# Optimization experiments

Hardware: AMD Instinct MI355X
Metric: run time of the kernel (lower is better)

The kernel has to match this reference:

```python
import jax, jax.numpy as jnp
import numpy as np

H = 64  # lstm_units
FORGET_BIAS = 1.0  # TF LSTMCell default


def setup_inputs() -> dict:
    key = jax.random.key(0)
    k1, k2, k3 = jax.random.split(key, 3)
    B, T = 256, 2048
    x = jax.random.normal(k1, (B, T, 1), dtype=jnp.float32)
    # Layer 1: LSTMCell(64), input dim 1 -> kernel [(1+64), 4*64]
    W1 = jax.random.normal(k2, (1 + H, 4 * H), dtype=jnp.float32) * 0.1
    b1 = jnp.zeros((4 * H,), dtype=jnp.float32)
    # Layer 2: LSTMCell(1), input dim 64 -> kernel [(64+1), 4*1]
    W2 = jax.random.normal(k3, (H + 1, 4), dtype=jnp.float32) * 0.1
    b2 = jnp.zeros((4,), dtype=jnp.float32)
    return {"x": x, "W1": W1, "b1": b1, "W2": W2, "b2": b2}


def _lstm_step(c, h, xt, W, b):
    # TF LSTMCell: gates from concat([x, h]) @ W + b, order i, j, f, o
    z = jnp.concatenate([xt, h], axis=-1) @ W + b
    i, j, f, o = jnp.split(z, 4, axis=-1)
    c_new = jax.nn.sigmoid(f + FORGET_BIAS) * c + jax.nn.sigmoid(i) * jnp.tanh(j)
    h_new = jax.nn.sigmoid(o) * jnpp_tanh(c_new) if False else jax.nn.sigmoid(o) * jnp.tanh(c_new)
    return c_new, h_new


def reference(x, W1, b1, W2, b2):
    # x: [B, T, 1] -> outputs of 2-layer stacked LSTM, final layer size 1
    B = x.shape[0]

    def step(carry, xt):
        c1, h1, c2, h2 = carry
        c1, h1 = _lstm_step(c1, h1, xt, W1, b1)
        c2, h2 = _lstm_step(c2, h2, h1, W2, b2)
        return (c1, h1, c2, h2), h2

    init = (
        jnp.zeros((B, H), x.dtype),
        jnp.zeros((B, H), x.dtype),
        jnp.zeros((B, 1), x.dtype),
        jnp.zeros((B, 1), x.dtype),
    )
    x_tbf = jnp.swapaxes(x, 0, 1)  # [T, B, 1]
    _, ys = jax.lax.scan(step, init, x_tbf)  # ys: [T, B, 1]
    return jnp.swapaxes(ys, 0, 1)  # [B, T, 1]
```

## Files before the change

kernel.cpp:

```cpp
#include <hip/hip_runtime.h>

constexpr int kT = 2048;
constexpr int kB = 256;
constexpr int kH = 64;

__device__ __forceinline__ float fast_sig(float x) {
    return __builtin_amdgcn_rcpf(1.0f + __expf(-x));
}
__device__ __forceinline__ float fast_tanh(float x) {
    float t = __expf(2.0f * x);
    return 1.0f - 2.0f * __builtin_amdgcn_rcpf(t + 1.0f);
}
__device__ __forceinline__ float bcast(float v, int lane) {
    return __int_as_float(__builtin_amdgcn_readlane(__float_as_int(v), lane));
}

__global__ __launch_bounds__(320)
__attribute__((amdgpu_waves_per_eu(1)))
void lstm2_kernel(
    const float* __restrict__ x, const float* __restrict__ W1,
    const float* __restrict__ b1, const float* __restrict__ W2,
    const float* __restrict__ b2, float* __restrict__ out)
{
    __shared__ float4 x4_lds[kT / 4];
    __shared__ float4 out4_lds[kT / 4];
    __shared__ float h1_lds[2][kH];
    float* x_lds = (float*)x4_lds;
    float* out_lds = (float*)out4_lds;

    const int tid = threadIdx.x;
    const int b = blockIdx.x;
    const float4* xg4 = (const float4*)(x + (size_t)b * kT);
    float4* outg4 = (float4*)(out + (size_t)b * kT);

    for (int i = tid; i < kT / 4; i += 320) x4_lds[i] = xg4[i];
    if (tid < kH) { h1_lds[0][tid] = 0.0f; h1_lds[1][tid] = 0.0f; }

    const int w = tid >> 6;
    const int l = tid & 63;

    float w0 = 0.0f, b1g = 0.0f;
    float4 wh4[16];
    #pragma unroll
    for (int k = 0; k < 16; ++k) wh4[k] = make_float4(0.f, 0.f, 0.f, 0.f);
    float c1 = 0.0f;
    int u = 0, g = 0;

    float w2p0 = 0, w2p1 = 0, w2p2 = 0, w2p3 = 0;
    float4 w2t = {0, 0, 0, 0}, b2v = {0, 0, 0, 0};
    float c2 = 0.0f, h2 = 0.0f;
    float zi_s = 0, zj_s = 0, zf_s = 0, zo_s = 0;

    if (w < 4) {
        g = l >> 4;
        u = 16 * w + (l & 15);
        const int col = g * 64 + u;
        w0 = W1[col];
        b1g = b1[col];
        #pragma unroll
        for (int k = 0; k < 16; ++k) {
            wh4[k].x = W1[(4 * k + 1) * 256 + col];
            wh4[k].y = W1[(4 * k + 2) * 256 + col];
            wh4[k].z = W1[(4 * k + 3) * 256 + col];
            wh4[k].w = W1[(4 * k + 4) * 256 + col];
        }
    } else {
        const int s = l & 15, gg = l >> 4;
        w2p0 = W2[(s +  0) * 4 + gg];
        w2p1 = W2[(s + 16) * 4 + gg];
        w2p2 = W2[(s + 32) * 4 + gg];
        w2p3 = W2[(s + 48) * 4 + gg];
        w2t = ((const float4*)W2)[kH];
        b2v = ((const float4*)b2)[0];
    }

    #pragma unroll
    for (int k = 0; k < 16; ++k)
        asm volatile("" : "+v"(wh4[k].x), "+v"(wh4[k].y),
                          "+v"(wh4[k].z), "+v"(wh4[k].w));
    asm volatile("" : "+v"(w0), "+v"(b1g));
    asm volatile("" : "+v"(w2p0), "+v"(w2p1), "+v"(w2p2), "+v"(w2p3));
    asm volatile("" : "+v"(w2t.x), "+v"(w2t.y), "+v"(w2t.z), "+v"(w2t.w));
    asm volatile("" : "+v"(b2v.x), "+v"(b2v.y), "+v"(b2v.z), "+v"(b2v.w));

    __syncthreads();

    int cur = 0;
    for (int t = 0; t < kT; ++t) {
        const int nxt = cur ^ 1;
        if (w < 4) {
            const float xt = x_lds[t];
            const float hv = h1_lds[cur][l];
            float z0 = fmaf(xt, w0, b1g), z1 = 0.0f, z2 = 0.0f, z3 = 0.0f;
            #pragma unroll
            for (int k = 0; k < 16; ++k) {
                z0 = fmaf(bcast(hv, 4 * k + 0), wh4[k].x, z0);
                z1 = fmaf(bcast(hv, 4 * k + 1), wh4[k].y, z1);
                z2 = fmaf(bcast(hv, 4 * k + 2), wh4[k].z, z2);
                z3 = fmaf(bcast(hv, 4 * k + 3), wh4[k].w, z3);
            }
            float z = (z0 + z1) + (z2 + z3);
            float zz = (g == 1) ? 2.0f * z : ((g == 2) ? z + 1.0f : z);
            float sg = fast_sig(zz);
            float a = (g == 1) ? fmaf(2.0f, sg, -1.0f) : sg;
            const int base = l & 15;
            const float ai = __shfl(a, base);
            const float aj = __shfl(a, base + 16);
            const float af = __shfl(a, base + 32);
            const float ao = __shfl(a, base + 48);
            c1 = fmaf(af, c1, ai * aj);
            const float h1n = ao * fast_tanh(c1);
            if (g == 0) h1_lds[nxt][u] = h1n;
        } else {
            if (t >= 2) {
                const float zi = zi_s + h2 * w2t.x;
                const float zj = zj_s + h2 * w2t.y;
                const float zf = zf_s + h2 * w2t.z;
                const float zo = zo_s + h2 * w2t.w;
                c2 = fast_sig(zf + 1.0f) * c2 + fast_sig(zi) * fast_tanh(zj);
                h2 = fast_sig(zo) * fast_tanh(c2);
                if (l == 0) out_lds[t - 2] = h2;
            }
            if (t >= 1) {
                const int s = l & 15;
                const float* hb = h1_lds[cur];
                float p = hb[s] * w2p0;
                p = fmaf(hb[s + 16], w2p1, p);
                p = fmaf(hb[s + 32], w2p2, p);
                p = fmaf(hb[s + 48], w2p3, p);
                p += __shfl_xor(p, 1);
                p += __shfl_xor(p, 2);
                p += __shfl_xor(p, 4);
                p += __shfl_xor(p, 8);
                zi_s = __shfl(p, s)      + b2v.x;
                zj_s = __shfl(p, s + 16) + b2v.y;
                zf_s = __shfl(p, s + 32) + b2v.z;
                zo_s = __shfl(p, s + 48) + b2v.w;
            }
        }
        __syncthreads();
        cur = nxt;
    }

    if (w == 4) {
        {
            const float zi = zi_s + h2 * w2t.x;
            const float zj = zj_s + h2 * w2t.y;
            const float zf = zf_s + h2 * w2t.z;
            const float zo = zo_s + h2 * w2t.w;
            c2 = fast_sig(zf + 1.0f) * c2 + fast_sig(zi) * fast_tanh(zj);
            h2 = fast_sig(zo) * fast_tanh(c2);
            if (l == 0) out_lds[kT - 2] = h2;
        }
        {
            const int s = l & 15;
            const float* hb = h1_lds[cur];
            float p = hb[s] * w2p0;
            p = fmaf(hb[s + 16], w2p1, p);
            p = fmaf(hb[s + 32], w2p2, p);
            p = fmaf(hb[s + 48], w2p3, p);
            p += __shfl_xor(p, 1);
            p += __shfl_xor(p, 2);
            p += __shfl_xor(p, 4);
            p += __shfl_xor(p, 8);
            const float zi = __shfl(p, s)      + b2v.x + h2 * w2t.x;
            const float zj = __shfl(p, s + 16) + b2v.y + h2 * w2t.y;
            const float zf = __shfl(p, s + 32) + b2v.z + h2 * w2t.z;
            const float zo = __shfl(p, s + 48) + b2v.w + h2 * w2t.w;
            c2 = fast_sig(zf + 1.0f) * c2 + fast_sig(zi) * fast_tanh(zj);
            h2 = fast_sig(zo) * fast_tanh(c2);
            if (l == 0) out_lds[kT - 1] = h2;
        }
    }

    __syncthreads();
    for (int i = tid; i < kT / 4; i += 320) outg4[i] = out4_lds[i];
}

extern "C" void kernel_launch(void* const* d_in, const int* in_sizes, int n_in,
                              void* d_out, int out_size, void* d_ws, size_t ws_size,
                              hipStream_t stream) {
    const float* x  = (const float*)d_in[0];
    const float* W1 = (const float*)d_in[1];
    const float* b1 = (const float*)d_in[2];
    const float* W2 = (const float*)d_in[3];
    const float* b2 = (const float*)d_in[4];
    float* out = (float*)d_out;
    lstm2_kernel<<<kB, 320, 0, stream>>>(x, W1, b1, W2, b2, out);
}
```

Measured before the change: 1.174 ms.

## Collapse LSTM recurrence to a single wavefront per batch row, removing block barriers

Each block now runs one 64-lane wavefront where every lane owns one hidden unit and holds all four gate columns (256 weights) in registers. The h state is broadcast through LDS as vector reads instead of readlane, and the gate dot products use packed two-wide float FMAs. Layer 2's input projection is reduced with DPP row adds and readlane, so the per-step __syncthreads across five waves goes away. The trade-off is very high VGPR pressure and a serial dependency chain inside one wave, which leaves little latency hiding.

```diff
diff --git a/kernel.cpp b/kernel.cpp
--- a/kernel.cpp
+++ b/kernel.cpp
@@ -3,6 +3,9 @@
 constexpr int kT = 2048;
 constexpr int kB = 256;
 constexpr int kH = 64;
+
+typedef __attribute__((ext_vector_type(2))) float f32x2;
+typedef __attribute__((ext_vector_type(4))) float f32x4;
 
 __device__ __forceinline__ float fast_sig(float x) {
     return __builtin_amdgcn_rcpf(1.0f + __expf(-x));
@@ -11,170 +14,127 @@
     float t = __expf(2.0f * x);
     return 1.0f - 2.0f * __builtin_amdgcn_rcpf(t + 1.0f);
 }
-__device__ __forceinline__ float bcast(float v, int lane) {
+__device__ __forceinline__ float rl(float v, int lane) {
     return __int_as_float(__builtin_amdgcn_readlane(__float_as_int(v), lane));
 }
+template <int CTRL>
+__device__ __forceinline__ float dpp_add(float v) {
+    int t = __builtin_amdgcn_update_dpp(0, __float_as_int(v), CTRL, 0xF, 0xF, true);
+    return v + __int_as_float(t);
+}
+__device__ __forceinline__ float row_reduce16(float v) {
+    v = dpp_add<0xB1>(v);
+    v = dpp_add<0x4E>(v);
+    v = dpp_add<0x141>(v);
+    v = dpp_add<0x140>(v);
+    return v;
+}
 
-__global__ __launch_bounds__(320)
+__global__ __launch_bounds__(64)
 __attribute__((amdgpu_waves_per_eu(1)))
 void lstm2_kernel(
     const float* __restrict__ x, const float* __restrict__ W1,
     const float* __restrict__ b1, const float* __restrict__ W2,
     const float* __restrict__ b2, float* __restrict__ out)
 {
-    __shared__ float4 x4_lds[kT / 4];
-    __shared__ float4 out4_lds[kT / 4];
-    __shared__ float h1_lds[2][kH];
+    __shared__ f32x4 x4_lds[kT / 4];
+    __shared__ f32x4 out4_lds[kT / 4];
+    __shared__ f32x4 h4_lds[kH / 4];
     float* x_lds = (float*)x4_lds;
     float* out_lds = (float*)out4_lds;
+    float* h_lds = (float*)h4_lds;
 
-    const int tid = threadIdx.x;
+    const int l = threadIdx.x;
     const int b = blockIdx.x;
-    const float4* xg4 = (const float4*)(x + (size_t)b * kT);
-    float4* outg4 = (float4*)(out + (size_t)b * kT);
+    const f32x4* xg4 = (const f32x4*)(x + (size_t)b * kT);
+    f32x4* outg4 = (f32x4*)(out + (size_t)b * kT);
 
-    for (int i = tid; i < kT / 4; i += 320) x4_lds[i] = xg4[i];
-    if (tid < kH) { h1_lds[0][tid] = 0.0f; h1_lds[1][tid] = 0.0f; }
+    for (int i = l; i < kT / 4; i += 64) x4_lds[i] = xg4[i];
+    h_lds[l] = 0.0f;
 
-    const int w = tid >> 6;
-    const int l = tid & 63;
+    f32x2 wp[4][32];
+    float w0g[4], bg[4], w2r[4];
+    #pragma unroll
+    for (int g = 0; g < 4; ++g) {
+        const int col = g * 64 + l;
+        w0g[g] = W1[col];
+        bg[g]  = b1[col];
+        #pragma unroll
+        for (int j = 0; j < 32; ++j) {
+            wp[g][j].x = W1[(2 * j + 1) * 256 + col];
+            wp[g][j].y = W1[(2 * j + 2) * 256 + col];
+        }
+        w2r[g] = W2[l * 4 + g];
+    }
+    f32x4 w2t = ((const f32x4*)W2)[kH];
+    f32x4 b2v = ((const f32x4*)b2)[0];
 
-    float w0 = 0.0f, b1g = 0.0f;
-    float4 wh4[16];
     #pragma unroll
-    for (int k = 0; k < 16; ++k) wh4[k] = make_float4(0.f, 0.f, 0.f, 0.f);
-    float c1 = 0.0f;
-    int u = 0, g = 0;
+    for (int g = 0; g < 4; ++g) {
+        #pragma unroll
+        for (int j = 0; j < 32; ++j) asm volatile("" : "+v"(wp[g][j]));
+        asm volatile("" : "+v"(w0g[g]), "+v"(bg[g]), "+v"(w2r[g]));
+    }
+    asm volatile("" : "+v"(w2t), "+v"(b2v));
 
-    float w2p0 = 0, w2p1 = 0, w2p2 = 0, w2p3 = 0;
-    float4 w2t = {0, 0, 0, 0}, b2v = {0, 0, 0, 0};
-    float c2 = 0.0f, h2 = 0.0f;
-    float zi_s = 0, zj_s = 0, zf_s = 0, zo_s = 0;
+    float c1 = 0.0f, h1own = 0.0f, c2 = 0.0f, h2 = 0.0f;
+    float r0 = 0.0f, r1 = 0.0f, r2 = 0.0f, r3 = 0.0f;
 
-    if (w < 4) {
-        g = l >> 4;
-        u = 16 * w + (l & 15);
-        const int col = g * 64 + u;
-        w0 = W1[col];
-        b1g = b1[col];
+    #pragma unroll 1
+    for (int t = 0; t < kT; ++t) {
+        const float xt = x_lds[t];
+        f32x4 h4[16];
+        #pragma unroll
+        for (int k = 0; k < 16; ++k) h4[k] = h4_lds[k];
+
+        if (t != 0) {
+            const float zi = rl(r0,0)+rl(r0,16)+rl(r0,32)+rl(r0,48) + b2v.x + h2 * w2t.x;
+            const float zj = rl(r1,0)+rl(r1,16)+rl(r1,32)+rl(r1,48) + b2v.y + h2 * w2t.y;
+            const float zf = rl(r2,0)+rl(r2,16)+rl(r2,32)+rl(r2,48) + b2v.z + h2 * w2t.z;
+            const float zo = rl(r3,0)+rl(r3,16)+rl(r3,32)+rl(r3,48) + b2v.w + h2 * w2t.w;
+            c2 = fast_sig(zf + 1.0f) * c2 + fast_sig(zi) * fast_tanh(zj);
+            h2 = fast_sig(zo) * fast_tanh(c2);
+            if (l == 0) out_lds[t - 1] = h2;
+        }
+
+        f32x2 a0 = {fmaf(xt, w0g[0], bg[0]), 0.0f};
+        f32x2 a1 = {fmaf(xt, w0g[1], bg[1]), 0.0f};
+        f32x2 a2 = {fmaf(xt, w0g[2], bg[2]), 0.0f};
+        f32x2 a3 = {fmaf(xt, w0g[3], bg[3]), 0.0f};
         #pragma unroll
         for (int k = 0; k < 16; ++k) {
-            wh4[k].x = W1[(4 * k + 1) * 256 + col];
-            wh4[k].y = W1[(4 * k + 2) * 256 + col];
-            wh4[k].z = W1[(4 * k + 3) * 256 + col];
-            wh4[k].w = W1[(4 * k + 4) * 256 + col];
+            const f32x2 lo = h4[k].xy;
+            const f32x2 hi = h4[k].zw;
+            a0 += lo * wp[0][2*k]; a0 += hi * wp[0][2*k+1];
+            a1 += lo * wp[1][2*k]; a1 += hi * wp[1][2*k+1];
+            a2 += lo * wp[2][2*k]; a2 += hi * wp[2][2*k+1];
+            a3 += lo * wp[3][2*k]; a3 += hi * wp[3][2*k+1];
         }
-    } else {
-        const int s = l & 15, gg = l >> 4;
-        w2p0 = W2[(s +  0) * 4 + gg];
-        w2p1 = W2[(s + 16) * 4 + gg];
-        w2p2 = W2[(s + 32) * 4 + gg];
-        w2p3 = W2[(s + 48) * 4 + gg];
-        w2t = ((const float4*)W2)[kH];
-        b2v = ((const float4*)b2)[0];
+        const float gi = fast_sig (a0.x + a0.y);
+        const float gj = fast_tanh(a1.x + a1.y);
+        const float gf = fast_sig (a2.x + a2.y + 1.0f);
+        const float go = fast_sig (a3.x + a3.y);
+        c1 = fmaf(gf, c1, gi * gj);
+        h1own = go * fast_tanh(c1);
+        h_lds[l] = h1own;
+
+        r0 = row_reduce16(h1own * w2r[0]);
+        r1 = row_reduce16(h1own * w2r[1]);
+        r2 = row_reduce16(h1own * w2r[2]);
+        r3 = row_reduce16(h1own * w2r[3]);
     }
 
-    #pragma unroll
-    for (int k = 0; k < 16; ++k)
-        asm volatile("" : "+v"(wh4[k].x), "+v"(wh4[k].y),
-                          "+v"(wh4[k].z), "+v"(wh4[k].w));
-    asm volatile("" : "+v"(w0), "+v"(b1g));
-    asm volatile("" : "+v"(w2p0), "+v"(w2p1), "+v"(w2p2), "+v"(w2p3));
-    asm volatile("" : "+v"(w2t.x), "+v"(w2t.y), "+v"(w2t.z), "+v"(w2t.w));
-    asm volatile("" : "+v"(b2v.x), "+v"(b2v.y), "+v"(b2v.z), "+v"(b2v.w));
-
-    __syncthreads();
-
-    int cur = 0;
-    for (int t = 0; t < kT; ++t) {
-        const int nxt = cur ^ 1;
-        if (w < 4) {
-            const float xt = x_lds[t];
-            const float hv = h1_lds[cur][l];
-            float z0 = fmaf(xt, w0, b1g), z1 = 0.0f, z2 = 0.0f, z3 = 0.0f;
-            #pragma unroll
-            for (int k = 0; k < 16; ++k) {
-                z0 = fmaf(bcast(hv, 4 * k + 0), wh4[k].x, z0);
-                z1 = fmaf(bcast(hv, 4 * k + 1), wh4[k].y, z1);
-                z2 = fmaf(bcast(hv, 4 * k + 2), wh4[k].z, z2);
-                z3 = fmaf(bcast(hv, 4 * k + 3), wh4[k].w, z3);
-            }
-            float z = (z0 + z1) + (z2 + z3);
-            float zz = (g == 1) ? 2.0f * z : ((g == 2) ? z + 1.0f : z);
-            float sg = fast_sig(zz);
-            float a = (g == 1) ? fmaf(2.0f, sg, -1.0f) : sg;
-            const int base = l & 15;
-            const float ai = __shfl(a, base);
-            const float aj = __shfl(a, base + 16);
-            const float af = __shfl(a, base + 32);
-            const float ao = __shfl(a, base + 48);
-            c1 = fmaf(af, c1, ai * aj);
-            const float h1n = ao * fast_tanh(c1);
-            if (g == 0) h1_lds[nxt][u] = h1n;
-        } else {
-            if (t >= 2) {
-                const float zi = zi_s + h2 * w2t.x;
-                const float zj = zj_s + h2 * w2t.y;
-                const float zf = zf_s + h2 * w2t.z;
-                const float zo = zo_s + h2 * w2t.w;
-                c2 = fast_sig(zf + 1.0f) * c2 + fast_sig(zi) * fast_tanh(zj);
-                h2 = fast_sig(zo) * fast_tanh(c2);
-                if (l == 0) out_lds[t - 2] = h2;
-            }
-            if (t >= 1) {
-                const int s = l & 15;
-                const float* hb = h1_lds[cur];
-                float p = hb[s] * w2p0;
-                p = fmaf(hb[s + 16], w2p1, p);
-                p = fmaf(hb[s + 32], w2p2, p);
-                p = fmaf(hb[s + 48], w2p3, p);
-                p += __shfl_xor(p, 1);
-                p += __shfl_xor(p, 2);
-                p += __shfl_xor(p, 4);
-                p += __shfl_xor(p, 8);
-                zi_s = __shfl(p, s)      + b2v.x;
-                zj_s = __shfl(p, s + 16) + b2v.y;
-                zf_s = __shfl(p, s + 32) + b2v.z;
-                zo_s = __shfl(p, s + 48) + b2v.w;
-            }
-        }
-        __syncthreads();
-        cur = nxt;
+    {
+        const float zi = rl(r0,0)+rl(r0,16)+rl(r0,32)+rl(r0,48) + b2v.x + h2 * w2t.x;
+        const float zj = rl(r1,0)+rl(r1,16)+rl(r1,32)+rl(r1,48) + b2v.y + h2 * w2t.y;
+        const float zf = rl(r2,0)+rl(r2,16)+rl(r2,32)+rl(r2,48) + b2v.z + h2 * w2t.z;
+        const float zo = rl(r3,0)+rl(r3,16)+rl(r3,32)+rl(r3,48) + b2v.w + h2 * w2t.w;
+        c2 = fast_sig(zf + 1.0f) * c2 + fast_sig(zi) * fast_tanh(zj);
+        h2 = fast_sig(zo) * fast_tanh(c2);
+        if (l == 0) out_lds[kT - 1] = h2;
     }
 
-    if (w == 4) {
-        {
-            const float zi = zi_s + h2 * w2t.x;
-            const float zj = zj_s + h2 * w2t.y;
-            const float zf = zf_s + h2 * w2t.z;
-            const float zo = zo_s + h2 * w2t.w;
-            c2 = fast_sig(zf + 1.0f) * c2 + fast_sig(zi) * fast_tanh(zj);
-            h2 = fast_sig(zo) * fast_tanh(c2);
-            if (l == 0) out_lds[kT - 2] = h2;
-        }
-        {
-            const int s = l & 15;
-            const float* hb = h1_lds[cur];
-            float p = hb[s] * w2p0;
-            p = fmaf(hb[s + 16], w2p1, p);
-            p = fmaf(hb[s + 32], w2p2, p);
-            p = fmaf(hb[s + 48], w2p3, p);
-            p += __shfl_xor(p, 1);
-            p += __shfl_xor(p, 2);
-            p += __shfl_xor(p, 4);
-            p += __shfl_xor(p, 8);
-            const float zi = __shfl(p, s)      + b2v.x + h2 * w2t.x;
-            const float zj = __shfl(p, s + 16) + b2v.y + h2 * w2t.y;
-            const float zf = __shfl(p, s + 32) + b2v.z + h2 * w2t.z;
-            const float zo = __shfl(p, s + 48) + b2v.w + h2 * w2t.w;
-            c2 = fast_sig(zf + 1.0f) * c2 + fast_sig(zi) * fast_tanh(zj);
-            h2 = fast_sig(zo) * fast_tanh(c2);
-            if (l == 0) out_lds[kT - 1] = h2;
-        }
-    }
-
-    __syncthreads();
-    for (int i = tid; i < kT / 4; i += 320) outg4[i] = out4_lds[i];
+    for (int i = l; i < kT / 4; i += 64) outg4[i] = out4_lds[i];
 }
 
 extern "C" void kernel_launch(void* const* d_in, const int* in_sizes, int n_in,
@@ -186,5 +146,5 @@
     const float* W2 = (const float*)d_in[3];
     const float* b2 = (const float*)d_in[4];
     float* out = (float*)d_out;
-    lstm2_kernel<<<kB, 320, 0, stream>>>(x, W1, b1, W2, b2, out);
+    lstm2_kernel<<<kB, 64, 0, stream>>>(x, W1, b1, W2, b2, out);
 }
```

Measured after the change: 1.753 ms. +49.3%, slower.
